# Kernel tuning notes

Measured on AMD Instinct MI355X. Metric: run time of the kernel, lower is better.

The kernel has to match this reference:

```python
import jax, jax.numpy as jnp
import numpy as np

C = 256
LN_EPS = 1e-5
LEAKY_SLOPE = 0.01

def _layernorm(t, g, b):
    mu = jnp.mean(t, axis=-1, keepdims=True)
    var = jnp.mean((t - mu) ** 2, axis=-1, keepdims=True)
    return (t - mu) * jax.lax.rsqrt(var + LN_EPS) * g + b

def setup_inputs() -> dict:
    key = jax.random.key(0)
    ks = jax.random.split(key, 16)
    b, d, h, w = 4, 4096, 64, 64
    s = lambda n: 1.0 / np.sqrt(n)
    return {
        "x": jax.random.normal(ks[0], (b, 1, d), jnp.float32),
        "y": jax.random.normal(ks[1], (b, C, h, w), jnp.float32),
        "q_w": jax.random.normal(ks[2], (C, C), jnp.float32) * s(C),
        "q_b": jnp.zeros((C,), jnp.float32),
        "dw_w": jax.random.normal(ks[3], (C,), jnp.float32),
        "dw_b": jnp.zeros((C,), jnp.float32),
        "kv_w1": jax.random.normal(ks[4], (1, C // 2), jnp.float32),
        "kv_b1": jnp.zeros((C // 2,), jnp.float32),
        "ln1_g": jnp.ones((C // 2,), jnp.float32),
        "ln1_b": jnp.zeros((C // 2,), jnp.float32),
        "kv_w2": jax.random.normal(ks[5], (C // 2, C), jnp.float32) * s(C // 2),
        "kv_b2": jnp.zeros((C,), jnp.float32),
        "ln2_g": jnp.ones((C,), jnp.float32),
        "ln2_b": jnp.zeros((C,), jnp.float32),
        "kv_w3": jax.random.normal(ks[6], (C, C), jnp.float32) * s(C),
        "kv_b3": jnp.zeros((C,), jnp.float32),
        "ln3_g": jnp.ones((C,), jnp.float32),
        "ln3_b": jnp.zeros((C,), jnp.float32),
        "kv_w4": jax.random.normal(ks[7], (C, 2 * C), jnp.float32) * s(C),
        "kv_b4": jnp.zeros((2 * C,), jnp.float32),
        "proj_w": jax.random.normal(ks[8], (C, C), jnp.float32) * s(C),
        "proj_b": jnp.zeros((C,), jnp.float32),
    }

def reference(x, y, q_w, q_b, dw_w, dw_b, kv_w1, kv_b1, ln1_g, ln1_b,
              kv_w2, kv_b2, ln2_g, ln2_b, kv_w3, kv_b3, ln3_g, ln3_b,
              kv_w4, kv_b4, proj_w, proj_b):
    b, c, h, w = y.shape
    # x: [b, 1, d] -> [b, d, 1]; MLP kv-generator lifts each scalar to 2c channels
    t = jnp.swapaxes(x, 1, 2)  # [b, d, 1]
    t = jax.nn.leaky_relu(_layernorm(t @ kv_w1 + kv_b1, ln1_g, ln1_b), LEAKY_SLOPE)
    t = jax.nn.leaky_relu(_layernorm(t @ kv_w2 + kv_b2, ln2_g, ln2_b), LEAKY_SLOPE)
    t = jax.nn.leaky_relu(_layernorm(t @ kv_w3 + kv_b3, ln3_g, ln3_b), LEAKY_SLOPE)
    t = jax.nn.silu(t @ kv_w4 + kv_b4)  # [b, d, 2c]
    k, v = jnp.split(t, 2, axis=-1)  # each [b, d, c]
    k = jnp.swapaxes(k, 1, 2)  # [b, c, d]
    # q = dwconv1x1(conv1x1(y)): 1x1 conv is a channel matmul; depthwise 1x1 is per-channel affine
    q = jnp.einsum('bchw,oc->bohw', y, q_w) + q_b[None, :, None, None]
    q = q * dw_w[None, :, None, None] + dw_b[None, :, None, None]
    q = q.reshape(b, c, h * w).transpose(0, 2, 1)  # [b, hw, c]
    scores = jnp.einsum('bic,bcd->bid', q, k) * (float(c) ** -0.5)  # [b, hw, d]
    attn = jax.nn.softmax(scores, axis=2)
    h_ = jnp.einsum('bid,bdc->bic', attn, v)  # [b, hw, c]
    h_ = h_.transpose(0, 2, 1).reshape(b, c, h, w)
    h_ = jnp.einsum('bchw,oc->bohw', h_, proj_w) + proj_b[None, :, None, None]
    return y + h_
```

## Files before the change

### kernel.cpp

```cpp
#include <hip/hip_runtime.h>
#include <cstdint>
#include <cstddef>

using bf16   = __bf16;
using bf16x8 = __bf16 __attribute__((ext_vector_type(8)));
using f32x4  = float  __attribute__((ext_vector_type(4)));
using u16    = unsigned short;
using ushort8 = __attribute__((ext_vector_type(8))) unsigned short;

#define MFMA16(a, b, c) __builtin_amdgcn_mfma_f32_16x16x32_bf16(a, b, c, 0, 0, 0)

__device__ __forceinline__ u16 f2bf(float f) {
  union { float f; unsigned u; } v; v.f = f;
  unsigned r = v.u + 0x7fffu + ((v.u >> 16) & 1u);
  return (u16)(r >> 16);
}
__device__ __forceinline__ u16 bfc(float f) {
  union { float f; unsigned u; } v; v.f = f;
  return (u16)((v.u + 0x8000u) >> 16);
}
__device__ __forceinline__ float b2f(u16 h) {
  union { unsigned u; float f; } v; v.u = ((unsigned)h) << 16; return v.f;
}
__device__ __forceinline__ bf16x8 ldb8(const u16* p) { return *(const bf16x8*)p; }
__device__ __forceinline__ float red_sum16(float v) {
  v += __shfl_xor(v, 1, 64); v += __shfl_xor(v, 2, 64);
  v += __shfl_xor(v, 4, 64); v += __shfl_xor(v, 8, 64);
  return v;
}
__device__ __forceinline__ void gll16(const u16* g, u16* l) {
  __builtin_amdgcn_global_load_lds(
      (const __attribute__((address_space(1))) void*)g,
      (__attribute__((address_space(3))) void*)l, 16, 0, 0);
}

#define QSCALE 0.09016844005556021f

__global__ void k_prep(const float* __restrict__ kv_w2, const float* __restrict__ kv_w3,
                       const float* __restrict__ kv_w4, const float* __restrict__ q_w,
                       const float* __restrict__ proj_w,
                       u16* __restrict__ Wt2, u16* __restrict__ Wt3, u16* __restrict__ Wt4,
                       u16* __restrict__ Qw, u16* __restrict__ Pww) {
  int idx = blockIdx.x * 256 + threadIdx.x;
  if (idx < 32768) {
    int n = idx >> 7, k = idx & 127;
    Wt2[idx] = f2bf(kv_w2[k * 256 + n]);
  } else if (idx < 98304) {
    int j = idx - 32768, n = j >> 8, k = j & 255;
    Wt3[j] = f2bf(kv_w3[k * 256 + n]);
  } else if (idx < 229376) {
    int j = idx - 98304, n = j >> 8, k = j & 255;
    Wt4[j] = f2bf(kv_w4[k * 512 + n]);
  } else if (idx < 294912) {
    int j = idx - 229376;
    Qw[j] = f2bf(q_w[j]);
  } else if (idx < 360448) {
    int j = idx - 294912;
    Pww[j] = f2bf(proj_w[j]);
  }
}

__device__ __forceinline__ void ln_store(f32x4* acc, const float* __restrict__ bias,
    const float* __restrict__ g, const float* __restrict__ bb, u16* act,
    int w, int quad, int l16) {
  #pragma unroll
  for (int f = 0; f < 16; ++f) {
    float bv = bias[f * 16 + l16];
    acc[f][0] += bv; acc[f][1] += bv; acc[f][2] += bv; acc[f][3] += bv;
  }
  #pragma unroll
  for (int r = 0; r < 4; ++r) {
    float s = 0;
    #pragma unroll
    for (int f = 0; f < 16; ++f) s += acc[f][r];
    s = red_sum16(s);
    float mu = s * (1.f / 256.f);
    float vv = 0;
    #pragma unroll
    for (int f = 0; f < 16; ++f) { float d = acc[f][r] - mu; vv += d * d; }
    vv = red_sum16(vv);
    float inv = rsqrtf(vv * (1.f / 256.f) + 1e-5f);
    int rl = w * 16 + quad * 4 + r;
    #pragma unroll
    for (int f = 0; f < 16; ++f) {
      int col = f * 16 + l16;
      float o = (acc[f][r] - mu) * inv * g[col] + bb[col];
      o = o > 0.f ? o : 0.01f * o;
      act[rl * 264 + col] = f2bf(o);
    }
  }
}

template<int K>
__device__ __forceinline__ void mlp_layer(u16* act, u16* sW, const u16* __restrict__ Wt,
    const float* __restrict__ bias, const float* __restrict__ g, const float* __restrict__ bb,
    int tid, int w, int quad, int l16) {
  bf16x8 af[K / 32];
  #pragma unroll
  for (int kk = 0; kk < K / 32; ++kk) af[kk] = ldb8(act + (w * 16 + l16) * 264 + kk * 32 + quad * 8);
  f32x4 z = {0.f, 0.f, 0.f, 0.f};
  f32x4 acc[16];
  #pragma unroll
  for (int f = 0; f < 16; ++f) acc[f] = z;
  for (int nc = 0; nc < 4; ++nc) {
    __syncthreads();
    #pragma unroll
    for (int p = 0; p < K / 32; ++p) {
      int q = p * 256 + tid; int row = q / (K / 8), c8 = q % (K / 8);
      *(uint4*)(sW + row * 264 + c8 * 8) = *(const uint4*)(Wt + (size_t)(nc * 64 + row) * K + c8 * 8);
    }
    __syncthreads();
    #pragma unroll
    for (int nb = 0; nb < 4; ++nb) {
      int f = nc * 4 + nb;
      #pragma unroll
      for (int kk = 0; kk < K / 32; ++kk)
        acc[f] = MFMA16(af[kk], ldb8(sW + (nb * 16 + l16) * 264 + kk * 32 + quad * 8), acc[f]);
    }
  }
  ln_store(acc, bias, g, bb, act, w, quad, l16);
  __syncthreads();
}

__device__ __forceinline__ void mlp_layer4(u16* act, u16* sW, const u16* __restrict__ Wt4,
    const float* __restrict__ bias4, u16* __restrict__ Kt, u16* __restrict__ Vt,
    int i0, int tid, int w, int quad, int l16) {
  bf16x8 af[8];
  #pragma unroll
  for (int kk = 0; kk < 8; ++kk) af[kk] = ldb8(act + (w * 16 + l16) * 264 + kk * 32 + quad * 8);
  f32x4 z = {0.f, 0.f, 0.f, 0.f};
  for (int h = 0; h < 2; ++h) {
    f32x4 acc[16];
    #pragma unroll
    for (int f = 0; f < 16; ++f) acc[f] = z;
    for (int nc = 0; nc < 4; ++nc) {
      __syncthreads();
      #pragma unroll
      for (int p = 0; p < 8; ++p) {
        int q = p * 256 + tid; int row = q >> 5, c8 = q & 31;
        *(uint4*)(sW + row * 264 + c8 * 8) =
            *(const uint4*)(Wt4 + (size_t)(h * 256 + nc * 64 + row) * 256 + c8 * 8);
      }
      __syncthreads();
      #pragma unroll
      for (int nb = 0; nb < 4; ++nb) {
        int f = nc * 4 + nb;
        #pragma unroll
        for (int kk = 0; kk < 8; ++kk)
          acc[f] = MFMA16(af[kk], ldb8(sW + (nb * 16 + l16) * 264 + kk * 32 + quad * 8), acc[f]);
      }
    }
    #pragma unroll
    for (int f = 0; f < 16; ++f) {
      int col = f * 16 + l16;
      float bv = bias4[h * 256 + col];
      if (h == 0) {
        int kk = f >> 1;
        int qs = (f & 1) * 2 + (l16 >> 3);
        int e  = l16 & 7;
        int l16base = (w & 1) * 8 + quad * 2;
        size_t tb = ((size_t)((i0 >> 5) + (w >> 1))) * 8192 + kk * 1024 + qs * 128 + e;
        #pragma unroll
        for (int r = 0; r < 4; ++r) {
          float v = acc[f][r] + bv;
          v = v / (1.f + __expf(-v));
          Kt[tb + (size_t)(r & 1) * 512 + (size_t)(l16base + (r >> 1)) * 8] = f2bf(v);
        }
      } else {
        int rowg0 = i0 + w * 16 + quad * 4;
        int bb2 = rowg0 >> 12;
        int tt = (rowg0 >> 5) & 127;
        int qv = (rowg0 >> 3) & 3;
        int e0 = rowg0 & 7;
        ushort4 u;
        #pragma unroll
        for (int r = 0; r < 4; ++r) {
          float v = acc[f][r] + bv;
          v = v / (1.f + __expf(-v));
          ((u16*)&u)[r] = f2bf(v);
        }
        size_t off = ((size_t)(bb2 * 128 + tt)) * 8192 + f * 512 + qv * 128 + l16 * 8 + e0;
        *(ushort4*)(Vt + off) = u;
      }
    }
  }
}

__global__ __launch_bounds__(256, 2) void k_fused(
    const float* __restrict__ x, const float* __restrict__ w1, const float* __restrict__ bias1,
    const float* __restrict__ g1, const float* __restrict__ bb1,
    const u16* __restrict__ Wt2, const float* __restrict__ bias2,
    const float* __restrict__ g2, const float* __restrict__ bb2,
    const u16* __restrict__ Wt3, const float* __restrict__ bias3,
    const float* __restrict__ g3, const float* __restrict__ bb3,
    const u16* __restrict__ Wt4, const float* __restrict__ bias4,
    const float* __restrict__ y, const u16* __restrict__ Qw,
    const float* __restrict__ qb, const float* __restrict__ dww, const float* __restrict__ dwb,
    u16* __restrict__ Kt, u16* __restrict__ Vt, u16* __restrict__ Qb) {
  __shared__ __align__(16) u16 smem[33792];
  int tid = threadIdx.x, w = tid >> 6, lane = tid & 63, quad = lane >> 4, l16 = lane & 15;

  if (blockIdx.x < 256) {
    u16* act = smem;
    u16* sW  = smem + 16896;
    int i0 = blockIdx.x * 64;
    {
      int rloc = w * 16 + (lane >> 2);
      int c0 = (lane & 3) * 32;
      float xv = x[i0 + rloc];
      float t[32];
      float s = 0.f;
      #pragma unroll
      for (int j = 0; j < 32; ++j) { t[j] = xv * w1[c0 + j] + bias1[c0 + j]; s += t[j]; }
      s += __shfl_xor(s, 1, 64); s += __shfl_xor(s, 2, 64);
      float mu = s * (1.f / 128.f);
      float vv = 0.f;
      #pragma unroll
      for (int j = 0; j < 32; ++j) { float d = t[j] - mu; vv += d * d; }
      vv += __shfl_xor(vv, 1, 64); vv += __shfl_xor(vv, 2, 64);
      float inv = rsqrtf(vv * (1.f / 128.f) + 1e-5f);
      #pragma unroll
      for (int jo = 0; jo < 4; ++jo) {
        ushort8 pk;
        #pragma unroll
        for (int e = 0; e < 8; ++e) {
          int j = jo * 8 + e;
          float o = (t[j] - mu) * inv * g1[c0 + j] + bb1[c0 + j];
          o = o > 0.f ? o : 0.01f * o;
          pk[e] = f2bf(o);
        }
        *(ushort8*)(act + rloc * 264 + c0 + jo * 8) = pk;
      }
    }
    __syncthreads();
    mlp_layer<128>(act, sW, Wt2, bias2, g2, bb2, tid, w, quad, l16);
    mlp_layer<256>(act, sW, Wt3, bias3, g3, bb3, tid, w, quad, l16);
    mlp_layer4(act, sW, Wt4, bias4, Kt, Vt, i0, tid, w, quad, l16);
    return;
  }

  u16* sY = smem;
  u16* sB = smem + 4608;
  int t = blockIdx.x - 256;
  int b = t >> 6, i0 = (t & 63) * 64;
  f32x4 z = {0.f, 0.f, 0.f, 0.f};
  f32x4 acc[16];
  #pragma unroll
  for (int f = 0; f < 16; ++f) acc[f] = z;
  for (int kc = 0; kc < 4; ++kc) {
    if (kc) __syncthreads();
    {
      int cl = tid >> 4;
      int il = (tid & 15) * 4;
      #pragma unroll
      for (int p = 0; p < 4; ++p) {
        int c = kc * 64 + p * 16 + cl;
        float4 v = *(const float4*)(y + ((size_t)(b * 256 + c)) * 4096 + i0 + il);
        sY[(il + 0) * 72 + p * 16 + cl] = f2bf(v.x);
        sY[(il + 1) * 72 + p * 16 + cl] = f2bf(v.y);
        sY[(il + 2) * 72 + p * 16 + cl] = f2bf(v.z);
        sY[(il + 3) * 72 + p * 16 + cl] = f2bf(v.w);
      }
    }
    #pragma unroll
    for (int p = 0; p < 8; ++p) {
      int q = p * 256 + tid; int row = q >> 3, k8 = q & 7;
      *(uint4*)(sB + row * 72 + k8 * 8) = *(const uint4*)(Qw + (size_t)row * 256 + kc * 64 + k8 * 8);
    }
    __syncthreads();
    #pragma unroll
    for (int kk = 0; kk < 2; ++kk) {
      bf16x8 af = ldb8(sY + (w * 16 + l16) * 72 + kk * 32 + quad * 8);
      #pragma unroll
      for (int f = 0; f < 16; ++f) {
        bf16x8 bfr = ldb8(sB + (f * 16 + l16) * 72 + kk * 32 + quad * 8);
        acc[f] = MFMA16(af, bfr, acc[f]);
      }
    }
  }
  #pragma unroll
  for (int f = 0; f < 16; ++f) {
    int col = f * 16 + l16;
    float q0 = qb[col], sc = dww[col], dB = dwb[col];
    #pragma unroll
    for (int r = 0; r < 4; ++r) {
      int rowg = i0 + w * 16 + quad * 4 + r;
      float v = ((acc[f][r] + q0) * sc + dB) * QSCALE;
      Qb[((size_t)(b * 4096 + rowg)) * 256 + col] = f2bf(v);
    }
  }
}

__global__ __launch_bounds__(256, 2) void k_attn(const u16* __restrict__ Qb, const u16* __restrict__ Kt,
    const u16* __restrict__ Vt, u16* __restrict__ Op, float* __restrict__ Ol) {
  __shared__ __align__(16) u16 smem[37888];
  int tid = threadIdx.x, w = tid >> 6, lane = tid & 63, quad = lane >> 4, l16 = lane & 15;
  int b = blockIdx.x & 3, kh = (blockIdx.x >> 2) & 3, qt = blockIdx.x >> 4;
  int i0 = qt * 128 + w * 32;

  bf16x8 qf[2][8];
  {
    const u16* qrow = Qb + ((size_t)(b * 4096 + i0 + l16)) * 256 + quad * 8;
    #pragma unroll
    for (int kk = 0; kk < 8; ++kk) {
      qf[0][kk] = ldb8(qrow + kk * 32);
      qf[1][kk] = ldb8(qrow + 16 * 256 + kk * 32);
    }
  }
  f32x4 z = {0.f, 0.f, 0.f, 0.f};
  f32x4 oacc[2][16];
  #pragma unroll
  for (int sub = 0; sub < 2; ++sub)
    #pragma unroll
    for (int f = 0; f < 16; ++f) oacc[sub][f] = z;
  float l4[2][4] = {{0.f, 0.f, 0.f, 0.f}, {0.f, 0.f, 0.f, 0.f}};

  u16* sPw = smem + 32768 + w * 1280;
  int wp = w & 1;
  const u16* gSrc = ((w < 2) ? Kt : Vt) + ((size_t)(b * 128 + kh * 32) * 8192) + wp * 4096 + lane * 8;
  u16* lBase = smem + ((w < 2) ? 0 : 8192) + wp * 4096 + lane * 8;

  #pragma unroll
  for (int i = 0; i < 8; ++i) gll16(gSrc + i * 512, lBase + i * 512);
  gSrc += 8192;

  #pragma unroll 1
  for (int kt = 0; kt < 32; ++kt) {
    int buf = kt & 1;
    const u16* sK = smem + buf * 16384;
    const u16* sV = sK + 8192;
    asm volatile("s_waitcnt vmcnt(0)" ::: "memory");
    __syncthreads();
    if (kt < 31) {
      u16* dst = lBase + (buf ^ 1) * 16384;
      #pragma unroll
      for (int i = 0; i < 8; ++i) gll16(gSrc + i * 512, dst + i * 512);
      gSrc += 8192;
    }
    f32x4 s00 = z, s01 = z, s10 = z, s11 = z;
    const u16* kb = sK + lane * 8;
    __builtin_amdgcn_s_setprio(1);
    #pragma unroll
    for (int kk = 0; kk < 8; ++kk) {
      bf16x8 k0 = ldb8(kb + kk * 1024);
      bf16x8 k1 = ldb8(kb + kk * 1024 + 512);
      s00 = MFMA16(qf[0][kk], k0, s00);
      s01 = MFMA16(qf[0][kk], k1, s01);
      s10 = MFMA16(qf[1][kk], k0, s10);
      s11 = MFMA16(qf[1][kk], k1, s11);
    }
    __builtin_amdgcn_s_setprio(0);
    #pragma unroll
    for (int r = 0; r < 4; ++r) {
      float p0 = exp2f(s00[r]);
      float p1 = exp2f(s01[r]);
      float p2 = exp2f(s10[r]);
      float p3 = exp2f(s11[r]);
      l4[0][r] += p0 + p1;
      l4[1][r] += p2 + p3;
      unsigned pk0 = ((unsigned)bfc(p1) << 16) | (unsigned)bfc(p0);
      unsigned pk1 = ((unsigned)bfc(p3) << 16) | (unsigned)bfc(p2);
      int row0 = (quad * 4 + r) * 40;
      *(unsigned*)(sPw + row0 + l16 * 2) = pk0;
      *(unsigned*)(sPw + 640 + row0 + l16 * 2) = pk1;
    }
    asm volatile("s_waitcnt lgkmcnt(0)" ::: "memory");
    bf16x8 pf0 = ldb8(sPw + l16 * 40 + quad * 8);
    bf16x8 pf1 = ldb8(sPw + 640 + l16 * 40 + quad * 8);
    const u16* vbase = sV + lane * 8;
    __builtin_amdgcn_s_setprio(1);
    #pragma unroll
    for (int f = 0; f < 16; ++f) {
      bf16x8 vf = ldb8(vbase + f * 512);
      oacc[0][f] = MFMA16(pf0, vf, oacc[0][f]);
      oacc[1][f] = MFMA16(pf1, vf, oacc[1][f]);
    }
    __builtin_amdgcn_s_setprio(0);
  }
  #pragma unroll
  for (int sub = 0; sub < 2; ++sub)
    #pragma unroll
    for (int r = 0; r < 4; ++r) l4[sub][r] = red_sum16(l4[sub][r]);
  #pragma unroll
  for (int sub = 0; sub < 2; ++sub)
    #pragma unroll
    for (int r = 0; r < 4; ++r) {
      size_t gr = (size_t)kh * 16384 + b * 4096 + i0 + sub * 16 + quad * 4 + r;
      u16* orow = Op + gr * 256;
      #pragma unroll
      for (int f = 0; f < 16; ++f) orow[f * 16 + l16] = f2bf(oacc[sub][f][r]);
      if (l16 == 0) Ol[gr] = l4[sub][r];
    }
}

__global__ __launch_bounds__(512) void k_proj(const u16* __restrict__ Op, const float* __restrict__ Ol,
    const u16* __restrict__ Pw, const float* __restrict__ pb, const float* __restrict__ y,
    float* __restrict__ out) {
  __shared__ __align__(16) u16 sA[128 * 136];
  __shared__ __align__(16) u16 sB[64 * 136];
  __shared__ float sW[64];
  int tid = threadIdx.x, w = tid >> 6, lane = tid & 63, quad = lane >> 4, l16 = lane & 15;
  int i0 = blockIdx.x * 64, o0 = blockIdx.y * 128, b = blockIdx.z;
  if (tid < 64) {
    size_t gr = (size_t)b * 4096 + i0 + tid;
    float L = Ol[gr] + Ol[gr + 16384] + Ol[gr + 32768] + Ol[gr + 49152];
    sW[tid] = 1.f / L;
  }
  __syncthreads();
  f32x4 z = {0.f, 0.f, 0.f, 0.f};
  f32x4 acc[4] = {z, z, z, z};
  for (int kc = 0; kc < 2; ++kc) {
    if (kc) __syncthreads();
    #pragma unroll
    for (int p = 0; p < 4; ++p) {
      int q = p * 512 + tid; int row = q >> 4, c8 = q & 15;
      *(uint4*)(sA + row * 136 + c8 * 8) = *(const uint4*)(Pw + ((size_t)(o0 + row)) * 256 + kc * 128 + c8 * 8);
    }
    #pragma unroll
    for (int p = 0; p < 2; ++p) {
      int q = p * 512 + tid; int row = q >> 4, c8 = q & 15;
      size_t gr = (size_t)b * 4096 + i0 + row;
      const u16* hp = Op + gr * 256 + kc * 128 + c8 * 8;
      uint4 u0 = *(const uint4*)(hp);
      uint4 u1 = *(const uint4*)(hp + 4194304);
      uint4 u2 = *(const uint4*)(hp + 8388608);
      uint4 u3 = *(const uint4*)(hp + 12582912);
      float wr = sW[row];
      const u16* p0 = (const u16*)&u0; const u16* p1 = (const u16*)&u1;
      const u16* p2 = (const u16*)&u2; const u16* p3 = (const u16*)&u3;
      ushort8 ov;
      #pragma unroll
      for (int e = 0; e < 8; ++e) {
        float v = (b2f(p0[e]) + b2f(p1[e]) + b2f(p2[e]) + b2f(p3[e])) * wr;
        ov[e] = f2bf(v);
      }
      *(ushort8*)(sB + row * 136 + c8 * 8) = ov;
    }
    __syncthreads();
    #pragma unroll
    for (int kk = 0; kk < 4; ++kk) {
      bf16x8 af = ldb8(sA + (w * 16 + l16) * 136 + kk * 32 + quad * 8);
      #pragma unroll
      for (int nb = 0; nb < 4; ++nb) {
        bf16x8 bfr = ldb8(sB + (nb * 16 + l16) * 136 + kk * 32 + quad * 8);
        acc[nb] = MFMA16(af, bfr, acc[nb]);
      }
    }
  }
  #pragma unroll
  for (int nb = 0; nb < 4; ++nb)
    #pragma unroll
    for (int r = 0; r < 4; ++r) {
      int og = o0 + w * 16 + quad * 4 + r;
      size_t idx = ((size_t)(b * 256 + og)) * 4096 + i0 + nb * 16 + l16;
      out[idx] = y[idx] + acc[nb][r] + pb[og];
    }
}

extern "C" void kernel_launch(void* const* d_in, const int* in_sizes, int n_in,
                              void* d_out, int out_size, void* d_ws, size_t ws_size,
                              hipStream_t stream) {
  (void)in_sizes; (void)n_in; (void)out_size; (void)ws_size;
  const float* x     = (const float*)d_in[0];
  const float* y     = (const float*)d_in[1];
  const float* q_w   = (const float*)d_in[2];
  const float* q_b   = (const float*)d_in[3];
  const float* dw_w  = (const float*)d_in[4];
  const float* dw_b  = (const float*)d_in[5];
  const float* kv_w1 = (const float*)d_in[6];
  const float* kv_b1 = (const float*)d_in[7];
  const float* ln1_g = (const float*)d_in[8];
  const float* ln1_b = (const float*)d_in[9];
  const float* kv_w2 = (const float*)d_in[10];
  const float* kv_b2 = (const float*)d_in[11];
  const float* ln2_g = (const float*)d_in[12];
  const float* ln2_b = (const float*)d_in[13];
  const float* kv_w3 = (const float*)d_in[14];
  const float* kv_b3 = (const float*)d_in[15];
  const float* ln3_g = (const float*)d_in[16];
  const float* ln3_b = (const float*)d_in[17];
  const float* kv_w4 = (const float*)d_in[18];
  const float* kv_b4 = (const float*)d_in[19];
  const float* proj_w = (const float*)d_in[20];
  const float* proj_b = (const float*)d_in[21];
  float* out = (float*)d_out;
  unsigned char* ws = (unsigned char*)d_ws;

  u16* Wt2 = (u16*)(ws + 0);
  u16* Wt3 = (u16*)(ws + 65536);
  u16* Wt4 = (u16*)(ws + 196608);
  u16* Qw  = (u16*)(ws + 458752);
  u16* Pww = (u16*)(ws + 589824);
  u16* Qb  = (u16*)(ws + 9437184);
  u16* Kt  = (u16*)(ws + 17825792);
  u16* Vt  = (u16*)(ws + 26214400);
  u16* Op  = (u16*)(ws + 34603008);
  float* Ol = (float*)(ws + 68157440);

  k_prep<<<1408, 256, 0, stream>>>(kv_w2, kv_w3, kv_w4, q_w, proj_w, Wt2, Wt3, Wt4, Qw, Pww);
  k_fused<<<512, 256, 0, stream>>>(x, kv_w1, kv_b1, ln1_g, ln1_b,
                                   Wt2, kv_b2, ln2_g, ln2_b,
                                   Wt3, kv_b3, ln3_g, ln3_b,
                                   Wt4, kv_b4,
                                   y, Qw, q_b, dw_w, dw_b,
                                   Kt, Vt, Qb);
  k_attn<<<512, 256, 0, stream>>>(Qb, Kt, Vt, Op, Ol);
  k_proj<<<dim3(64, 2, 4), 512, 0, stream>>>(Op, Ol, Pww, proj_b, y, out);
}
```

Before: 230.3 us.

## Pre-swizzle proj weights into MFMA fragment order and retile projection kernel

The prep kernel now stores the projection weights in MFMA A-fragment order, so each lane in k_proj loads its fragment directly from global memory instead of staging weights through shared memory. k_proj is retiled to 32 spatial rows by all 256 output channels per block. The combined-head O tile is merged once per block over the full K=256, which removes the second K-chunk and its barriers and stops recomputing the head merge for each output-channel half. The cost is more global weight reads per block, served from L2, and smaller spatial tiles, which give shorter 32-float output row segments.

```diff
diff --git a/kernel.cpp b/kernel.cpp
--- a/kernel.cpp
+++ b/kernel.cpp
@@ -55,8 +55,9 @@
     int j = idx - 229376;
     Qw[j] = f2bf(q_w[j]);
   } else if (idx < 360448) {
-    int j = idx - 294912;
-    Pww[j] = f2bf(proj_w[j]);
+    int j = idx - 294912, e = j & 7, l = (j >> 3) & 63, t = j >> 9;
+    int k8 = t & 7, f = t >> 3;
+    Pww[j] = f2bf(proj_w[(f * 16 + (l & 15)) * 256 + k8 * 32 + (l >> 4) * 8 + e]);
   }
 }
 
@@ -394,67 +395,64 @@
 }
 
 __global__ __launch_bounds__(512) void k_proj(const u16* __restrict__ Op, const float* __restrict__ Ol,
-    const u16* __restrict__ Pw, const float* __restrict__ pb, const float* __restrict__ y,
+    const u16* __restrict__ Pf, const float* __restrict__ pb, const float* __restrict__ y,
     float* __restrict__ out) {
-  __shared__ __align__(16) u16 sA[128 * 136];
-  __shared__ __align__(16) u16 sB[64 * 136];
-  __shared__ float sW[64];
+  __shared__ __align__(16) u16 sB[32 * 264];
+  __shared__ float sW[32];
   int tid = threadIdx.x, w = tid >> 6, lane = tid & 63, quad = lane >> 4, l16 = lane & 15;
-  int i0 = blockIdx.x * 64, o0 = blockIdx.y * 128, b = blockIdx.z;
-  if (tid < 64) {
+  int i0 = blockIdx.x * 32, b = blockIdx.y;
+  if (tid < 32) {
     size_t gr = (size_t)b * 4096 + i0 + tid;
     float L = Ol[gr] + Ol[gr + 16384] + Ol[gr + 32768] + Ol[gr + 49152];
     sW[tid] = 1.f / L;
   }
   __syncthreads();
+  #pragma unroll
+  for (int p = 0; p < 2; ++p) {
+    int q = p * 512 + tid; int row = q >> 5, c8 = q & 31;
+    size_t gr = (size_t)b * 4096 + i0 + row;
+    const u16* hp = Op + gr * 256 + c8 * 8;
+    uint4 u0 = *(const uint4*)(hp);
+    uint4 u1 = *(const uint4*)(hp + 4194304);
+    uint4 u2 = *(const uint4*)(hp + 8388608);
+    uint4 u3 = *(const uint4*)(hp + 12582912);
+    float wr = sW[row];
+    const u16* p0 = (const u16*)&u0; const u16* p1 = (const u16*)&u1;
+    const u16* p2 = (const u16*)&u2; const u16* p3 = (const u16*)&u3;
+    ushort8 ov;
+    #pragma unroll
+    for (int e = 0; e < 8; ++e) {
+      float v = (b2f(p0[e]) + b2f(p1[e]) + b2f(p2[e]) + b2f(p3[e])) * wr;
+      ov[e] = f2bf(v);
+    }
+    *(ushort8*)(sB + row * 264 + c8 * 8) = ov;
+  }
+  __syncthreads();
   f32x4 z = {0.f, 0.f, 0.f, 0.f};
-  f32x4 acc[4] = {z, z, z, z};
-  for (int kc = 0; kc < 2; ++kc) {
-    if (kc) __syncthreads();
-    #pragma unroll
-    for (int p = 0; p < 4; ++p) {
-      int q = p * 512 + tid; int row = q >> 4, c8 = q & 15;
-      *(uint4*)(sA + row * 136 + c8 * 8) = *(const uint4*)(Pw + ((size_t)(o0 + row)) * 256 + kc * 128 + c8 * 8);
-    }
-    #pragma unroll
-    for (int p = 0; p < 2; ++p) {
-      int q = p * 512 + tid; int row = q >> 4, c8 = q & 15;
-      size_t gr = (size_t)b * 4096 + i0 + row;
-      const u16* hp = Op + gr * 256 + kc * 128 + c8 * 8;
-      uint4 u0 = *(const uint4*)(hp);
-      uint4 u1 = *(const uint4*)(hp + 4194304);
-      uint4 u2 = *(const uint4*)(hp + 8388608);
-      uint4 u3 = *(const uint4*)(hp + 12582912);
-      float wr = sW[row];
-      const u16* p0 = (const u16*)&u0; const u16* p1 = (const u16*)&u1;
-      const u16* p2 = (const u16*)&u2; const u16* p3 = (const u16*)&u3;
-      ushort8 ov;
-      #pragma unroll
-      for (int e = 0; e < 8; ++e) {
-        float v = (b2f(p0[e]) + b2f(p1[e]) + b2f(p2[e]) + b2f(p3[e])) * wr;
-        ov[e] = f2bf(v);
-      }
-      *(ushort8*)(sB + row * 136 + c8 * 8) = ov;
-    }
-    __syncthreads();
-    #pragma unroll
-    for (int kk = 0; kk < 4; ++kk) {
-      bf16x8 af = ldb8(sA + (w * 16 + l16) * 136 + kk * 32 + quad * 8);
-      #pragma unroll
-      for (int nb = 0; nb < 4; ++nb) {
-        bf16x8 bfr = ldb8(sB + (nb * 16 + l16) * 136 + kk * 32 + quad * 8);
-        acc[nb] = MFMA16(af, bfr, acc[nb]);
-      }
-    }
-  }
-  #pragma unroll
-  for (int nb = 0; nb < 4; ++nb)
-    #pragma unroll
-    for (int r = 0; r < 4; ++r) {
-      int og = o0 + w * 16 + quad * 4 + r;
-      size_t idx = ((size_t)(b * 256 + og)) * 4096 + i0 + nb * 16 + l16;
-      out[idx] = y[idx] + acc[nb][r] + pb[og];
-    }
+  f32x4 acc[2][2] = {{z, z}, {z, z}};
+  const u16* pf0 = Pf + (size_t)((w * 2 + 0) * 8 * 64 + lane) * 8;
+  const u16* pf1 = Pf + (size_t)((w * 2 + 1) * 8 * 64 + lane) * 8;
+  #pragma unroll
+  for (int kk = 0; kk < 8; ++kk) {
+    bf16x8 b0 = ldb8(sB + l16 * 264 + kk * 32 + quad * 8);
+    bf16x8 b1 = ldb8(sB + (16 + l16) * 264 + kk * 32 + quad * 8);
+    bf16x8 a0 = ldb8(pf0 + (size_t)kk * 512);
+    bf16x8 a1 = ldb8(pf1 + (size_t)kk * 512);
+    acc[0][0] = MFMA16(a0, b0, acc[0][0]);
+    acc[0][1] = MFMA16(a0, b1, acc[0][1]);
+    acc[1][0] = MFMA16(a1, b0, acc[1][0]);
+    acc[1][1] = MFMA16(a1, b1, acc[1][1]);
+  }
+  #pragma unroll
+  for (int oc = 0; oc < 2; ++oc)
+    #pragma unroll
+    for (int nb = 0; nb < 2; ++nb)
+      #pragma unroll
+      for (int r = 0; r < 4; ++r) {
+        int og = w * 32 + oc * 16 + quad * 4 + r;
+        size_t idx = ((size_t)(b * 256 + og)) * 4096 + i0 + nb * 16 + l16;
+        out[idx] = y[idx] + acc[oc][nb][r] + pb[og];
+      }
 }
 
 extern "C" void kernel_launch(void* const* d_in, const int* in_sizes, int n_in,
@@ -505,5 +503,5 @@
                                    y, Qw, q_b, dw_w, dw_b,
                                    Kt, Vt, Qb);
   k_attn<<<512, 256, 0, stream>>>(Qb, Kt, Vt, Op, Ol);
-  k_proj<<<dim3(64, 2, 4), 512, 0, stream>>>(Op, Ol, Pww, proj_b, y, out);
-}
+  k_proj<<<dim3(128, 4), 512, 0, stream>>>(Op, Ol, Pww, proj_b, y, out);
+}
```

New measurement: 230.4 us, median of 2. About the same (+0.0%).
